# Optimization experiments

Hardware: AMD Instinct MI355X
Metric: run time of the kernel (lower is better)

The kernel has to match this reference:

```python
import jax, jax.numpy as jnp
import numpy as np

TEMPERATURE = 0.1
NEG_INF = -1e30  # finite sentinel to keep logsumexp grad-safe


def setup_inputs() -> dict:
    key = jax.random.key(0)
    k_emb, k_lab = jax.random.split(key)
    B, D, C = 8192, 256, 100
    embeddings = jax.random.normal(k_emb, (B, D), dtype=jnp.float32)
    labels = jax.random.randint(k_lab, (B,), 0, C, dtype=jnp.int64)
    return {"embeddings": embeddings, "labels": labels}


def reference(embeddings, labels):
    B = embeddings.shape[0]
    # squared L2 pairwise distance: ||x_i||^2 + ||x_j||^2 - 2 x_i . x_j
    sq = jnp.sum(embeddings * embeddings, axis=1)  # [B]
    gram = jnp.einsum('id,jd->ij', embeddings, embeddings)  # [B,B]
    dist2 = jnp.maximum(sq[:, None] + sq[None, :] - 2.0 * gram, 0.0)
    sim = -dist2 / TEMPERATURE  # [B,B]

    same = labels[:, None] == labels[None, :]
    eye = jnp.eye(B, dtype=bool)
    pos_mask = same & ~eye
    neg_mask = ~same

    # per-row uniform random positive via Gumbel-argmax over pos_mask
    k_sel = jax.random.key(42)
    g = jax.random.gumbel(k_sel, (B, B), dtype=jnp.float32)
    j = jnp.argmax(jnp.where(pos_mask, g, -jnp.inf), axis=1)  # [B]

    numerator = jnp.take_along_axis(sim, j[:, None], axis=1)[:, 0]  # sim[i, j_i]
    denominator = jax.nn.logsumexp(jnp.where(neg_mask, sim, NEG_INF), axis=1)

    valid = pos_mask.any(axis=1) & neg_mask.any(axis=1)
    per_row = -(numerator - denominator)
    n_valid = jnp.sum(valid)
    loss = jnp.sum(jnp.where(valid, per_row, 0.0)) / jnp.maximum(n_valid, 1)
    return jnp.where(n_valid > 0, loss, 0.0)
```

## Files before the change

### kernel.cpp

```cpp
#include <hip/hip_runtime.h>
#include <float.h>
#include <math.h>


#define B_N 8192
#define D_K 256
#define NCLS 100
#define MAXC 512
#define NSPLIT 16
#define NPART NSPLIT
#define JR (B_N / NSPLIT)
#define BI 128
#define BJ 128
#define NJT (JR / BJ)
#define BK 64
#define NKC (D_K / BK)
#define NEG_INF -1e30f

typedef __attribute__((ext_vector_type(8))) short bf16x8;
typedef __attribute__((ext_vector_type(4))) float f32x4;
typedef unsigned short ushort_t;

__device__ __forceinline__ unsigned rotl32(unsigned x, int d){ return (x << d) | (x >> (32 - d)); }

__device__ __forceinline__ float gumbel_at(unsigned idx){
  const unsigned HALF = (unsigned)B_N * (unsigned)B_N / 2u;
  unsigned c0, c1; bool second;
  if (idx < HALF){ c0 = idx; c1 = idx + HALF; second = false; }
  else            { c0 = idx - HALF; c1 = idx; second = true; }
  const unsigned ks0 = 0u, ks1 = 42u, ks2 = 0u ^ 42u ^ 0x1BD11BDAu;
  unsigned x0 = c0 + ks0, x1 = c1 + ks1;
#define TF_RND(r) { x0 += x1; x1 = rotl32(x1, (r)); x1 ^= x0; }
  TF_RND(13) TF_RND(15) TF_RND(26) TF_RND(6)   x0 += ks1; x1 += ks2 + 1u;
  TF_RND(17) TF_RND(29) TF_RND(16) TF_RND(24)  x0 += ks2; x1 += ks0 + 2u;
  TF_RND(13) TF_RND(15) TF_RND(26) TF_RND(6)   x0 += ks0; x1 += ks1 + 3u;
  TF_RND(17) TF_RND(29) TF_RND(16) TF_RND(24)  x0 += ks1; x1 += ks2 + 4u;
  TF_RND(13) TF_RND(15) TF_RND(26) TF_RND(6)   x0 += ks2; x1 += ks0 + 5u;
#undef TF_RND
  unsigned bits = second ? x1 : x0;
  float u = __uint_as_float((bits >> 9) | 0x3f800000u) - 1.0f;
  const float TINY = 1.17549435e-38f;
  u = u * (1.0f - TINY) + TINY;
  u = fmaxf(TINY, u);
  return -logf(-logf(u));
}

__device__ __forceinline__ ushort_t f2bf(float x){
  unsigned u = __float_as_uint(x);
  return (ushort_t)((u + 0x7FFFu + ((u >> 16) & 1u)) >> 16);
}

__device__ __forceinline__ void async16(const ushort_t* g, ushort_t* lds_wave_base){
  __builtin_amdgcn_global_load_lds((const __attribute__((address_space(1))) void*)g,
                                   (__attribute__((address_space(3))) void*)lds_wave_base,
                                   16, 0, 0);
}

__global__ void prep_kernel(const float* __restrict__ E, ushort_t* __restrict__ Ebf,
                            float* __restrict__ sq, float* __restrict__ acc4){
  if (blockIdx.x == 0 && threadIdx.x < 4)
    acc4[threadIdx.x] = 0.f;
  int w = threadIdx.x >> 6, lane = threadIdx.x & 63;
  int row = blockIdx.x * 4 + w;
  const float4 v = *reinterpret_cast<const float4*>(E + (size_t)row * D_K + lane * 4);
  float s = v.x*v.x + v.y*v.y + v.z*v.z + v.w*v.w;
#pragma unroll
  for (int off = 32; off > 0; off >>= 1) s += __shfl_down(s, off);
  if (lane == 0) sq[row] = s;
  ushort4 o; o.x = f2bf(v.x); o.y = f2bf(v.y); o.z = f2bf(v.z); o.w = f2bf(v.w);
  *reinterpret_cast<ushort4*>(Ebf + (size_t)row * D_K + lane * 4) = o;
}

__global__ __launch_bounds__(256)
void classsel_kernel(const int* __restrict__ labels, int* __restrict__ jsel){
  __shared__ int s_list[MAXC];
  __shared__ int s_n;
  const int c = blockIdx.x;
  const int tid = threadIdx.x;
  if (tid == 0) s_n = 0;
  __syncthreads();
  for (int t = tid; t < B_N; t += 256){
    if (labels[t] == c){
      int p = atomicAdd(&s_n, 1);
      if (p < MAXC) s_list[p] = t;
    }
  }
  __syncthreads();
  const int n = min(s_n, MAXC);
  for (int rowIdx = tid; rowIdx < n; rowIdx += 256){
    const int row = s_list[rowIdx];
    float gb = -FLT_MAX; int jb = -1;
    for (int t = 0; t < n; t++){
      int j = s_list[t];
      if (j != row){
        float g = gumbel_at(((unsigned)row << 13) + (unsigned)j);
        if (g > gb || (g == gb && (unsigned)j < (unsigned)jb)){ gb = g; jb = j; }
      }
    }
    jsel[row] = jb;
  }
}

__global__ __launch_bounds__(256, 2)
void fused_kernel(const ushort_t* __restrict__ Ebf, const int* __restrict__ labels,
                  const float* __restrict__ sq, const int* __restrict__ jsel,
                  float* __restrict__ numer,
                  float* __restrict__ wsM, float* __restrict__ wsS)
{
  __shared__ __align__(16) ushort_t Bs[NKC][BJ * BK];
  __shared__ float s_sqj[JR];
  __shared__ int   s_lj[JR];
  __shared__ float s_sqi[BI];
  __shared__ int   s_li[BI];
  __shared__ int   s_ji[BI];

  const int bi    = blockIdx.x >> 4;
  const int split = blockIdx.x & 15;
  const int i0    = bi * BI;
  const int jbase = split * JR;
  const int tid   = threadIdx.x;
  const int lane  = tid & 63;
  const int w     = tid >> 6;
  const int quad  = lane >> 4;
  const int l15   = lane & 15;

  for (int t = tid; t < JR; t += 256){ s_sqj[t] = sq[jbase + t]; s_lj[t] = labels[jbase + t]; }
  if (tid < BI){ s_sqi[tid] = sq[i0 + tid]; s_li[tid] = labels[i0 + tid]; s_ji[tid] = jsel[i0 + tid]; }

  bf16x8 af[2][8];
#pragma unroll
  for (int mt = 0; mt < 2; mt++){
    const ushort_t* rp = Ebf + (size_t)(i0 + w * 32 + mt * 16 + l15) * D_K + quad * 8;
#pragma unroll
    for (int c = 0; c < 8; c++)
      af[mt][c] = *reinterpret_cast<const bf16x8*>(rp + c * 32);
  }

  float sm[8], ssum[8];
#pragma unroll
  for (int r = 0; r < 8; r++){ sm[r] = NEG_INF; ssum[r] = 0.f; }

  __syncthreads();

  for (int jt = 0; jt < NJT; jt++){
    const int j0 = jbase + jt * BJ;
    f32x4 acc[2][8];
#pragma unroll
    for (int mt = 0; mt < 2; mt++)
#pragma unroll
      for (int nt = 0; nt < 8; nt++) acc[mt][nt] = (f32x4)0.f;

    __syncthreads();
#pragma unroll
    for (int kc = 0; kc < NKC; kc++){
#pragma unroll
      for (int rd = 0; rd < 4; rd++){
        int slot = rd * 256 + tid;
        int r = slot >> 3, gs = slot & 7;
        int gsrc = (gs ^ (r & 7)) << 3;
        ushort_t* ldsB = &Bs[kc][(size_t)(rd * 256 + w * 64) * 8];
        async16(Ebf + (size_t)(j0 + r) * D_K + kc * BK + gsrc, ldsB);
      }
    }
    __syncthreads();

#pragma unroll
    for (int kc = 0; kc < NKC; kc++){
#pragma unroll
      for (int s = 0; s < 2; s++){
        const int g = s * 4 + quad;
        const int c = kc * 2 + s;
        bf16x8 bfr[8];
#pragma unroll
        for (int nt = 0; nt < 8; nt++){
          int r = nt * 16 + l15;
          bfr[nt] = *reinterpret_cast<const bf16x8*>(&Bs[kc][r * BK + ((g ^ (r & 7)) << 3)]);
        }
#pragma unroll
        for (int nt = 0; nt < 8; nt++){
          acc[0][nt] = __builtin_amdgcn_mfma_f32_16x16x32_bf16(af[0][c], bfr[nt], acc[0][nt], 0, 0, 0);
          acc[1][nt] = __builtin_amdgcn_mfma_f32_16x16x32_bf16(af[1][c], bfr[nt], acc[1][nt], 0, 0, 0);
        }
      }
    }

    float sqj[8]; int lj[8];
#pragma unroll
    for (int nt = 0; nt < 8; nt++){
      int ccol = jt * BJ + nt * 16 + l15;
      sqj[nt] = s_sqj[ccol]; lj[nt] = s_lj[ccol];
    }
#pragma unroll
    for (int mt = 0; mt < 2; mt++){
#pragma unroll
      for (int rr = 0; rr < 4; rr++){
        int rl = w * 32 + mt * 16 + quad * 4 + rr;
        float sqv = s_sqi[rl]; int lrow = s_li[rl]; int jsl = s_ji[rl];
        int sidx = mt * 4 + rr;
        float sv[8];
#pragma unroll
        for (int nt = 0; nt < 8; nt++){
          float a = acc[mt][nt][rr];
          float simv = -10.f * fmaxf(fmaf(-2.f, a, sqv + sqj[nt]), 0.f);
          int colg = j0 + nt * 16 + l15;
          if (colg == jsl) numer[i0 + rl] = simv;
          sv[nt] = (lj[nt] != lrow) ? simv : NEG_INF;
        }
        float m8 = fmaxf(fmaxf(fmaxf(sv[0],sv[1]),fmaxf(sv[2],sv[3])),
                         fmaxf(fmaxf(sv[4],sv[5]),fmaxf(sv[6],sv[7])));
        float s8 = __expf(sv[0]-m8)+__expf(sv[1]-m8)+__expf(sv[2]-m8)+__expf(sv[3]-m8)
                 + __expf(sv[4]-m8)+__expf(sv[5]-m8)+__expf(sv[6]-m8)+__expf(sv[7]-m8);
        float M = fmaxf(sm[sidx], m8);
        ssum[sidx] = ssum[sidx]*__expf(sm[sidx]-M) + s8*__expf(m8-M);
        sm[sidx] = M;
      }
    }
  }

#pragma unroll
  for (int sidx = 0; sidx < 8; sidx++){
    float mv = sm[sidx], sv2 = ssum[sidx];
#pragma unroll
    for (int mask = 1; mask < 16; mask <<= 1){
      float m2 = __shfl_xor(mv, mask);
      float s2 = __shfl_xor(sv2, mask);
      float M = fmaxf(mv, m2);
      sv2 = sv2 * __expf(mv - M) + s2 * __expf(m2 - M);
      mv = M;
    }
    if (l15 == 0){
      int mt = sidx >> 2, rr = sidx & 3;
      int rl = w * 32 + mt * 16 + quad * 4 + rr;
      int o = split * B_N + i0 + rl;
      wsM[o] = mv; wsS[o] = sv2;
    }
  }
}

__global__ __launch_bounds__(256)
void finale_kernel(const float* __restrict__ wsM, const float* __restrict__ wsS,
                   const float* __restrict__ numer, const int* __restrict__ jsel,
                   float* __restrict__ acc4, float* __restrict__ out)
{
  const int tid = threadIdx.x;
  const int row = blockIdx.x * 256 + tid;
  float M = -3.0e38f, S = 0.f;
#pragma unroll
  for (int p = 0; p < NPART; p++){
    float m2 = wsM[p * B_N + row], s2 = wsS[p * B_N + row];
    float Mn = fmaxf(M, m2);
    S = S * __expf(M - Mn) + s2 * __expf(m2 - Mn);
    M = Mn;
  }
  bool v = (jsel[row] >= 0) && (M > -5e29f);
  float s = v ? (M + logf(S) - numer[row]) : 0.f;
  unsigned n = v ? 1u : 0u;
#pragma unroll
  for (int off = 32; off > 0; off >>= 1){ s += __shfl_down(s, off); n += __shfl_down(n, off); }
  __shared__ float ssm[4]; __shared__ unsigned snm[4];
  if ((tid & 63) == 0){ ssm[tid >> 6] = s; snm[tid >> 6] = n; }
  __syncthreads();
  if (tid == 0){
    float bs = ssm[0] + ssm[1] + ssm[2] + ssm[3];
    unsigned bn = snm[0] + snm[1] + snm[2] + snm[3];
    atomicAdd(&acc4[0], bs);
    atomicAdd((unsigned*)&acc4[1], bn);
    __threadfence();
    unsigned old = atomicAdd((unsigned*)&acc4[2], 1u);
    if (old == 31u){
      float St = atomicAdd(&acc4[0], 0.f);
      unsigned Nt = atomicAdd((unsigned*)&acc4[1], 0u);
      out[0] = (Nt > 0u) ? (St / (float)Nt) : 0.f;
    }
  }
}

extern "C" void kernel_launch(void* const* d_in, const int* in_sizes, int n_in,
                              void* d_out, int out_size, void* d_ws, size_t ws_size,
                              hipStream_t stream)
{
  const float* E      = (const float*)d_in[0];
  const int*   labels = (const int*)d_in[1];
  float*       out    = (float*)d_out;

  ushort_t* Ebf = (ushort_t*)d_ws;
  float* wsM    = (float*)(Ebf + (size_t)B_N * D_K);
  float* wsS    = wsM + NPART * B_N;
  float* sqb    = wsS + NPART * B_N;
  float* numer  = sqb + B_N;
  int* jsel     = (int*)(numer + B_N);
  float* acc4   = (float*)(jsel + B_N);

  prep_kernel<<<B_N / 4, 256, 0, stream>>>(E, Ebf, sqb, acc4);
  classsel_kernel<<<NCLS, 256, 0, stream>>>(labels, jsel);
  fused_kernel<<<(B_N / BI) * NSPLIT, 256, 0, stream>>>(Ebf, labels, sqb, jsel, numer, wsM, wsS);
  finale_kernel<<<B_N / 256, 256, 0, stream>>>(wsM, wsS, numer, jsel, acc4, out);
}
```

Measured before the change: 164.8 us.

## Double-buffer B tiles, halve row tile, parallelize positive selection, use base-2 exp

The fused kernel now streams the B operand through a two-slot LDS ring, issuing the next k-chunk's async loads while MFMAs run on the current one. The row tile shrinks from 128 to 64 rows and occupancy hints rise to 4 blocks per CU, which gives more blocks and waves to hide latency. Positive selection moves from one-thread-per-row loops inside per-class blocks to a wave-per-row reduction, and class-list building is folded into the prep kernel. Softmax math works in the log2 domain with native exp2/log2 and pre-scaled norms. This adds a barrier per k-chunk and halves A-operand reuse per B tile, so total B traffic through LDS doubles.

```diff
diff --git a/kernel.cpp b/kernel.cpp
--- a/kernel.cpp
+++ b/kernel.cpp
@@ -10,16 +10,22 @@
 #define NSPLIT 16
 #define NPART NSPLIT
 #define JR (B_N / NSPLIT)
-#define BI 128
+#define BI 64
 #define BJ 128
 #define NJT (JR / BJ)
 #define BK 64
 #define NKC (D_K / BK)
 #define NEG_INF -1e30f
+#define C2F  (-14.426950408889634f)
+#define K2A  (28.853900817779268f)
+#define LN2F (0.6931471805599453f)
 
 typedef __attribute__((ext_vector_type(8))) short bf16x8;
 typedef __attribute__((ext_vector_type(4))) float f32x4;
 typedef unsigned short ushort_t;
+
+__device__ __forceinline__ float ex2(float x){ return __builtin_amdgcn_exp2f(x); }
+__device__ __forceinline__ float lg2(float x){ return __builtin_amdgcn_logf(x); }
 
 __device__ __forceinline__ unsigned rotl32(unsigned x, int d){ return (x << d) | (x >> (32 - d)); }
 
@@ -56,61 +62,76 @@
                                    16, 0, 0);
 }
 
-__global__ void prep_kernel(const float* __restrict__ E, ushort_t* __restrict__ Ebf,
-                            float* __restrict__ sq, float* __restrict__ acc4){
-  if (blockIdx.x == 0 && threadIdx.x < 4)
-    acc4[threadIdx.x] = 0.f;
-  int w = threadIdx.x >> 6, lane = threadIdx.x & 63;
-  int row = blockIdx.x * 4 + w;
-  const float4 v = *reinterpret_cast<const float4*>(E + (size_t)row * D_K + lane * 4);
-  float s = v.x*v.x + v.y*v.y + v.z*v.z + v.w*v.w;
-#pragma unroll
-  for (int off = 32; off > 0; off >>= 1) s += __shfl_down(s, off);
-  if (lane == 0) sq[row] = s;
-  ushort4 o; o.x = f2bf(v.x); o.y = f2bf(v.y); o.z = f2bf(v.z); o.w = f2bf(v.w);
-  *reinterpret_cast<ushort4*>(Ebf + (size_t)row * D_K + lane * 4) = o;
-}
-
 __global__ __launch_bounds__(256)
-void classsel_kernel(const int* __restrict__ labels, int* __restrict__ jsel){
+void prep_kernel(const float* __restrict__ E, ushort_t* __restrict__ Ebf,
+                 float* __restrict__ sq, float* __restrict__ acc4,
+                 const int* __restrict__ labels, int* __restrict__ cls_cnt,
+                 int* __restrict__ clist){
   __shared__ int s_list[MAXC];
   __shared__ int s_n;
-  const int c = blockIdx.x;
-  const int tid = threadIdx.x;
-  if (tid == 0) s_n = 0;
-  __syncthreads();
-  for (int t = tid; t < B_N; t += 256){
-    if (labels[t] == c){
-      int p = atomicAdd(&s_n, 1);
-      if (p < MAXC) s_list[p] = t;
-    }
-  }
-  __syncthreads();
-  const int n = min(s_n, MAXC);
-  for (int rowIdx = tid; rowIdx < n; rowIdx += 256){
-    const int row = s_list[rowIdx];
-    float gb = -FLT_MAX; int jb = -1;
-    for (int t = 0; t < n; t++){
-      int j = s_list[t];
-      if (j != row){
-        float g = gumbel_at(((unsigned)row << 13) + (unsigned)j);
-        if (g > gb || (g == gb && (unsigned)j < (unsigned)jb)){ gb = g; jb = j; }
+  if (blockIdx.x < B_N / 4){
+    if (blockIdx.x == 0 && threadIdx.x < 4) acc4[threadIdx.x] = 0.f;
+    int w = threadIdx.x >> 6, lane = threadIdx.x & 63;
+    int row = blockIdx.x * 4 + w;
+    const float4 v = *reinterpret_cast<const float4*>(E + (size_t)row * D_K + lane * 4);
+    float s = v.x*v.x + v.y*v.y + v.z*v.z + v.w*v.w;
+#pragma unroll
+    for (int off = 32; off > 0; off >>= 1) s += __shfl_down(s, off);
+    if (lane == 0) sq[row] = s;
+    ushort4 o; o.x = f2bf(v.x); o.y = f2bf(v.y); o.z = f2bf(v.z); o.w = f2bf(v.w);
+    *reinterpret_cast<ushort4*>(Ebf + (size_t)row * D_K + lane * 4) = o;
+  } else {
+    const int c = blockIdx.x - B_N / 4;
+    const int tid = threadIdx.x;
+    if (tid == 0) s_n = 0;
+    __syncthreads();
+    for (int t = tid; t < B_N; t += 256){
+      if (labels[t] == c){
+        int p = atomicAdd(&s_n, 1);
+        if (p < MAXC) s_list[p] = t;
       }
     }
-    jsel[row] = jb;
-  }
-}
-
-__global__ __launch_bounds__(256, 2)
+    __syncthreads();
+    const int n = min(s_n, MAXC);
+    if (tid == 0) cls_cnt[c] = n;
+    for (int t = tid; t < n; t += 256) clist[c * MAXC + t] = s_list[t];
+  }
+}
+
+__global__ __launch_bounds__(256)
+void rowsel_kernel(const int* __restrict__ labels, const int* __restrict__ cls_cnt,
+                   const int* __restrict__ clist, int* __restrict__ jsel){
+  const int w = threadIdx.x >> 6, lane = threadIdx.x & 63;
+  const int row = blockIdx.x * 4 + w;
+  const int c = labels[row];
+  const int n = min(cls_cnt[c], MAXC);
+  float gb = -FLT_MAX; int jb = -1;
+  for (int t = lane; t < n; t += 64){
+    int j = clist[c * MAXC + t];
+    if (j != row){
+      float g = gumbel_at(((unsigned)row << 13) + (unsigned)j);
+      if (g > gb || (g == gb && (unsigned)j < (unsigned)jb)){ gb = g; jb = j; }
+    }
+  }
+#pragma unroll
+  for (int off = 32; off > 0; off >>= 1){
+    float g2 = __shfl_down(gb, off);
+    int   j2 = __shfl_down(jb, off);
+    if (g2 > gb || (g2 == gb && (unsigned)j2 < (unsigned)jb)){ gb = g2; jb = j2; }
+  }
+  if (lane == 0) jsel[row] = jb;
+}
+
+__global__ __launch_bounds__(256, 4)
 void fused_kernel(const ushort_t* __restrict__ Ebf, const int* __restrict__ labels,
                   const float* __restrict__ sq, const int* __restrict__ jsel,
                   float* __restrict__ numer,
                   float* __restrict__ wsM, float* __restrict__ wsS)
 {
-  __shared__ __align__(16) ushort_t Bs[NKC][BJ * BK];
-  __shared__ float s_sqj[JR];
+  __shared__ __align__(16) ushort_t Bs[2][BJ * BK];
+  __shared__ float s_h2j[JR];
   __shared__ int   s_lj[JR];
-  __shared__ float s_sqi[BI];
+  __shared__ float s_h2i[BI];
   __shared__ int   s_li[BI];
   __shared__ int   s_ji[BI];
 
@@ -124,113 +145,119 @@
   const int quad  = lane >> 4;
   const int l15   = lane & 15;
 
-  for (int t = tid; t < JR; t += 256){ s_sqj[t] = sq[jbase + t]; s_lj[t] = labels[jbase + t]; }
-  if (tid < BI){ s_sqi[tid] = sq[i0 + tid]; s_li[tid] = labels[i0 + tid]; s_ji[tid] = jsel[i0 + tid]; }
-
-  bf16x8 af[2][8];
-#pragma unroll
-  for (int mt = 0; mt < 2; mt++){
-    const ushort_t* rp = Ebf + (size_t)(i0 + w * 32 + mt * 16 + l15) * D_K + quad * 8;
+  for (int t = tid; t < JR; t += 256){ s_h2j[t] = C2F * sq[jbase + t]; s_lj[t] = labels[jbase + t]; }
+  if (tid < BI){ s_h2i[tid] = C2F * sq[i0 + tid]; s_li[tid] = labels[i0 + tid]; s_ji[tid] = jsel[i0 + tid]; }
+
+  bf16x8 af[8];
+  {
+    const ushort_t* rp = Ebf + (size_t)(i0 + w * 16 + l15) * D_K + quad * 8;
 #pragma unroll
     for (int c = 0; c < 8; c++)
-      af[mt][c] = *reinterpret_cast<const bf16x8*>(rp + c * 32);
-  }
-
-  float sm[8], ssum[8];
-#pragma unroll
-  for (int r = 0; r < 8; r++){ sm[r] = NEG_INF; ssum[r] = 0.f; }
-
+      af[c] = *reinterpret_cast<const bf16x8*>(rp + c * 32);
+  }
+
+  f32x4 acc[8];
+#pragma unroll
+  for (int nt = 0; nt < 8; nt++) acc[nt] = (f32x4)0.f;
+  float sm[4], ssum[4];
+#pragma unroll
+  for (int r = 0; r < 4; r++){ sm[r] = NEG_INF; ssum[r] = 0.f; }
+
+  int soff[4];
+#pragma unroll
+  for (int rd = 0; rd < 4; rd++){
+    int slot = rd * 256 + tid;
+    int r = slot >> 3, gs = slot & 7;
+    soff[rd] = r * D_K + ((gs ^ (r & 7)) << 3);
+  }
+
+#pragma unroll
+  for (int rd = 0; rd < 4; rd++)
+    async16(Ebf + (size_t)jbase * D_K + soff[rd],
+            &Bs[0][(size_t)(rd * 256 + w * 64) * 8]);
   __syncthreads();
 
+#pragma unroll 1
   for (int jt = 0; jt < NJT; jt++){
     const int j0 = jbase + jt * BJ;
-    f32x4 acc[2][8];
-#pragma unroll
-    for (int mt = 0; mt < 2; mt++)
-#pragma unroll
-      for (int nt = 0; nt < 8; nt++) acc[mt][nt] = (f32x4)0.f;
-
-    __syncthreads();
 #pragma unroll
     for (int kc = 0; kc < NKC; kc++){
-#pragma unroll
-      for (int rd = 0; rd < 4; rd++){
-        int slot = rd * 256 + tid;
-        int r = slot >> 3, gs = slot & 7;
-        int gsrc = (gs ^ (r & 7)) << 3;
-        ushort_t* ldsB = &Bs[kc][(size_t)(rd * 256 + w * 64) * 8];
-        async16(Ebf + (size_t)(j0 + r) * D_K + kc * BK + gsrc, ldsB);
+      const int b = kc & 1;
+      const int sn = jt * NKC + kc + 1;
+      if (sn < NJT * NKC){
+        const int kcn = sn & 3;
+        const size_t gb0 = (size_t)(jbase + (sn >> 2) * BJ) * D_K + (size_t)kcn * BK;
+#pragma unroll
+        for (int rd = 0; rd < 4; rd++)
+          async16(Ebf + gb0 + soff[rd],
+                  &Bs[b ^ 1][(size_t)(rd * 256 + w * 64) * 8]);
       }
-    }
-    __syncthreads();
-
-#pragma unroll
-    for (int kc = 0; kc < NKC; kc++){
 #pragma unroll
       for (int s = 0; s < 2; s++){
         const int g = s * 4 + quad;
         const int c = kc * 2 + s;
-        bf16x8 bfr[8];
-#pragma unroll
-        for (int nt = 0; nt < 8; nt++){
-          int r = nt * 16 + l15;
-          bfr[nt] = *reinterpret_cast<const bf16x8*>(&Bs[kc][r * BK + ((g ^ (r & 7)) << 3)]);
-        }
-#pragma unroll
-        for (int nt = 0; nt < 8; nt++){
-          acc[0][nt] = __builtin_amdgcn_mfma_f32_16x16x32_bf16(af[0][c], bfr[nt], acc[0][nt], 0, 0, 0);
-          acc[1][nt] = __builtin_amdgcn_mfma_f32_16x16x32_bf16(af[1][c], bfr[nt], acc[1][nt], 0, 0, 0);
+#pragma unroll
+        for (int h = 0; h < 2; h++){
+          bf16x8 bfr[4];
+#pragma unroll
+          for (int q = 0; q < 4; q++){
+            int r = (h * 4 + q) * 16 + l15;
+            bfr[q] = *reinterpret_cast<const bf16x8*>(&Bs[b][r * BK + ((g ^ (r & 7)) << 3)]);
+          }
+#pragma unroll
+          for (int q = 0; q < 4; q++)
+            acc[h * 4 + q] = __builtin_amdgcn_mfma_f32_16x16x32_bf16(af[c], bfr[q], acc[h * 4 + q], 0, 0, 0);
         }
       }
-    }
-
-    float sqj[8]; int lj[8];
-#pragma unroll
-    for (int nt = 0; nt < 8; nt++){
-      int ccol = jt * BJ + nt * 16 + l15;
-      sqj[nt] = s_sqj[ccol]; lj[nt] = s_lj[ccol];
-    }
-#pragma unroll
-    for (int mt = 0; mt < 2; mt++){
-#pragma unroll
-      for (int rr = 0; rr < 4; rr++){
-        int rl = w * 32 + mt * 16 + quad * 4 + rr;
-        float sqv = s_sqi[rl]; int lrow = s_li[rl]; int jsl = s_ji[rl];
-        int sidx = mt * 4 + rr;
-        float sv[8];
+      if (kc == NKC - 1){
+        float h2j[8]; int lj[8];
 #pragma unroll
         for (int nt = 0; nt < 8; nt++){
-          float a = acc[mt][nt][rr];
-          float simv = -10.f * fmaxf(fmaf(-2.f, a, sqv + sqj[nt]), 0.f);
-          int colg = j0 + nt * 16 + l15;
-          if (colg == jsl) numer[i0 + rl] = simv;
-          sv[nt] = (lj[nt] != lrow) ? simv : NEG_INF;
+          int ccol = jt * BJ + nt * 16 + l15;
+          h2j[nt] = s_h2j[ccol]; lj[nt] = s_lj[ccol];
         }
-        float m8 = fmaxf(fmaxf(fmaxf(sv[0],sv[1]),fmaxf(sv[2],sv[3])),
-                         fmaxf(fmaxf(sv[4],sv[5]),fmaxf(sv[6],sv[7])));
-        float s8 = __expf(sv[0]-m8)+__expf(sv[1]-m8)+__expf(sv[2]-m8)+__expf(sv[3]-m8)
-                 + __expf(sv[4]-m8)+__expf(sv[5]-m8)+__expf(sv[6]-m8)+__expf(sv[7]-m8);
-        float M = fmaxf(sm[sidx], m8);
-        ssum[sidx] = ssum[sidx]*__expf(sm[sidx]-M) + s8*__expf(m8-M);
-        sm[sidx] = M;
+#pragma unroll
+        for (int rr = 0; rr < 4; rr++){
+          const int rl = w * 16 + quad * 4 + rr;
+          const float h2i = s_h2i[rl];
+          const int lrow = s_li[rl], jsl = s_ji[rl];
+          float sv[8];
+#pragma unroll
+          for (int nt = 0; nt < 8; nt++){
+            float a = acc[nt][rr];
+            float sim2 = fminf(fmaf(K2A, a, h2i + h2j[nt]), 0.f);
+            int colg = j0 + nt * 16 + l15;
+            if (colg == jsl) numer[i0 + rl] = sim2;
+            sv[nt] = (lj[nt] != lrow) ? sim2 : NEG_INF;
+          }
+          float m8 = fmaxf(fmaxf(fmaxf(sv[0],sv[1]),fmaxf(sv[2],sv[3])),
+                           fmaxf(fmaxf(sv[4],sv[5]),fmaxf(sv[6],sv[7])));
+          float s8 = ex2(sv[0]-m8)+ex2(sv[1]-m8)+ex2(sv[2]-m8)+ex2(sv[3]-m8)
+                   + ex2(sv[4]-m8)+ex2(sv[5]-m8)+ex2(sv[6]-m8)+ex2(sv[7]-m8);
+          float M = fmaxf(sm[rr], m8);
+          ssum[rr] = ssum[rr]*ex2(sm[rr]-M) + s8*ex2(m8-M);
+          sm[rr] = M;
+        }
+#pragma unroll
+        for (int nt = 0; nt < 8; nt++) acc[nt] = (f32x4)0.f;
       }
-    }
-  }
-
-#pragma unroll
-  for (int sidx = 0; sidx < 8; sidx++){
-    float mv = sm[sidx], sv2 = ssum[sidx];
+      __syncthreads();
+    }
+  }
+
+#pragma unroll
+  for (int rr = 0; rr < 4; rr++){
+    float mv = sm[rr], sv2 = ssum[rr];
 #pragma unroll
     for (int mask = 1; mask < 16; mask <<= 1){
       float m2 = __shfl_xor(mv, mask);
       float s2 = __shfl_xor(sv2, mask);
       float M = fmaxf(mv, m2);
-      sv2 = sv2 * __expf(mv - M) + s2 * __expf(m2 - M);
+      sv2 = sv2 * ex2(mv - M) + s2 * ex2(m2 - M);
       mv = M;
     }
     if (l15 == 0){
-      int mt = sidx >> 2, rr = sidx & 3;
-      int rl = w * 32 + mt * 16 + quad * 4 + rr;
+      int rl = w * 16 + quad * 4 + rr;
       int o = split * B_N + i0 + rl;
       wsM[o] = mv; wsS[o] = sv2;
     }
@@ -249,11 +276,11 @@
   for (int p = 0; p < NPART; p++){
     float m2 = wsM[p * B_N + row], s2 = wsS[p * B_N + row];
     float Mn = fmaxf(M, m2);
-    S = S * __expf(M - Mn) + s2 * __expf(m2 - Mn);
+    S = S * ex2(M - Mn) + s2 * ex2(m2 - Mn);
     M = Mn;
   }
   bool v = (jsel[row] >= 0) && (M > -5e29f);
-  float s = v ? (M + logf(S) - numer[row]) : 0.f;
+  float s = v ? (LN2F * (M + lg2(S) - numer[row])) : 0.f;
   unsigned n = v ? 1u : 0u;
 #pragma unroll
   for (int off = 32; off > 0; off >>= 1){ s += __shfl_down(s, off); n += __shfl_down(n, off); }
@@ -290,9 +317,11 @@
   float* numer  = sqb + B_N;
   int* jsel     = (int*)(numer + B_N);
   float* acc4   = (float*)(jsel + B_N);
-
-  prep_kernel<<<B_N / 4, 256, 0, stream>>>(E, Ebf, sqb, acc4);
-  classsel_kernel<<<NCLS, 256, 0, stream>>>(labels, jsel);
+  int* cls_cnt  = (int*)(acc4 + 4);
+  int* clist    = cls_cnt + NCLS;
+
+  prep_kernel<<<B_N / 4 + NCLS, 256, 0, stream>>>(E, Ebf, sqb, acc4, labels, cls_cnt, clist);
+  rowsel_kernel<<<B_N / 4, 256, 0, stream>>>(labels, cls_cnt, clist, jsel);
   fused_kernel<<<(B_N / BI) * NSPLIT, 256, 0, stream>>>(Ebf, labels, sqb, jsel, numer, wsM, wsS);
   finale_kernel<<<B_N / 256, 256, 0, stream>>>(wsM, wsS, numer, jsel, acc4, out);
 }
```

Result: faster. 133.6 us (-19.0%).
